# Kernel optimization log

Hardware: AMD Instinct MI355X
Metric: run time of the kernel (lower is better)

## Reference

```python
import jax, jax.numpy as jnp
import numpy as np

N_LAYERS = 12
N_CH = 256
N_IN = 4
KS = 3
SPECT_CH = 640


def conv1d(x, w, b, dilation):
    # x: [B, T, Cin], w: [K, Cin, Cout] (WIO), SAME padding, given dilation
    y = jax.lax.conv_general_dilated(
        x, w, window_strides=(1,), padding='SAME',
        rhs_dilation=(dilation,), dimension_numbers=('NWC', 'WIO', 'NWC'))
    return y + b


def setup_inputs() -> dict:
    key = jax.random.key(0)
    ks = jax.random.split(key, 16)
    s = 0.02
    inp = {}
    inp['audio'] = jax.random.normal(ks[0], (8, 4096, N_IN), dtype=jnp.float32)
    inp['spect'] = jax.random.normal(ks[1], (8, 4096, SPECT_CH), dtype=jnp.float32)
    # start 1x1 conv: [Cin, Cout]
    inp['w_start'] = jax.random.normal(ks[2], (N_IN, N_CH), dtype=jnp.float32) * s
    inp['b_start'] = jnp.zeros((N_CH,), dtype=jnp.float32)
    # dilated in_layers: stacked [L, K, Cin, 2*Cout]
    inp['w_in'] = jax.random.normal(ks[3], (N_LAYERS, KS, N_CH, 2 * N_CH), dtype=jnp.float32) * s
    inp['b_in'] = jnp.zeros((N_LAYERS, 2 * N_CH), dtype=jnp.float32)
    # cond 1x1 convs: stacked [L, SPECT_CH, 2*Cout]
    inp['w_cond'] = jax.random.normal(ks[4], (N_LAYERS, SPECT_CH, 2 * N_CH), dtype=jnp.float32) * s
    inp['b_cond'] = jnp.zeros((N_LAYERS, 2 * N_CH), dtype=jnp.float32)
    # res_skip 1x1 convs: first L-1 have 2*Cout, last has Cout
    inp['w_res'] = jax.random.normal(ks[5], (N_LAYERS - 1, N_CH, 2 * N_CH), dtype=jnp.float32) * s
    inp['b_res'] = jnp.zeros((N_LAYERS - 1, 2 * N_CH), dtype=jnp.float32)
    inp['w_res_last'] = jax.random.normal(ks[6], (N_CH, N_CH), dtype=jnp.float32) * s
    inp['b_res_last'] = jnp.zeros((N_CH,), dtype=jnp.float32)
    # end 1x1 conv (zero-initialized in the original; use small random for a
    # non-degenerate numerical baseline)
    inp['w_end'] = jax.random.normal(ks[7], (N_CH, 2 * N_IN), dtype=jnp.float32) * s
    inp['b_end'] = jnp.zeros((2 * N_IN,), dtype=jnp.float32)
    return inp


def reference(audio, spect, w_start, b_start, w_in, b_in, w_cond, b_cond,
              w_res, b_res, w_res_last, b_res_last, w_end, b_end):
    # start: 1x1 conv == matmul over channels
    started = jnp.einsum('btc,cd->btd', audio, w_start) + b_start  # [B,T,256]
    # precompute all conditioning projections: [L,B,T,512]
    cond_all = jnp.einsum('btc,lcd->lbtd', spect, w_cond) + b_cond[:, None, None, :]
    output = None
    for i in range(N_LAYERS):
        in_l = conv1d(started, w_in[i], b_in[i], 2 ** i)  # [B,T,512]
        acts = in_l + cond_all[i]
        half_tanh = jnp.tanh(acts[..., :N_CH])
        half_sig = jax.nn.sigmoid(acts[..., N_CH:])
        activated = half_tanh * half_sig  # [B,T,256]
        if i < N_LAYERS - 1:
            rs = jnp.einsum('btc,cd->btd', activated, w_res[i]) + b_res[i]
            started = started + rs[..., :N_CH]
            skip = rs[..., N_CH:]
        else:
            skip = jnp.einsum('btc,cd->btd', activated, w_res_last) + b_res_last
        output = skip if output is None else output + skip
    out = jnp.einsum('btc,cd->btd', output, w_end) + b_end  # [B,T,2*N_IN]
    return out
```

## Files before the change

### kernel.cpp

```cpp
#include <hip/hip_runtime.h>
#include <cstdint>

#define PAD 2048
#define KG 1408

typedef float f32x4 __attribute__((ext_vector_type(4)));
typedef __bf16 bf16x8 __attribute__((ext_vector_type(8)));
typedef __bf16 bf16x4 __attribute__((ext_vector_type(4)));

__device__ __forceinline__ void g2l16(const void* g, void* l) {
    __builtin_amdgcn_global_load_lds(
        (__attribute__((address_space(1))) void*)(uintptr_t)g,
        (__attribute__((address_space(3))) void*)(uint32_t)(uintptr_t)l,
        16, 0, 0);
}


__global__ void cvt_bf16_kernel(const float4* __restrict__ src, bf16x4* __restrict__ dst, int n4) {
    int idx = blockIdx.x * 256 + threadIdx.x;
    if (idx < n4) {
        float4 v = src[idx];
        bf16x4 o = {(__bf16)v.x, (__bf16)v.y, (__bf16)v.z, (__bf16)v.w};
        dst[idx] = o;
    }
}

__global__ void init_started_kernel(const float* __restrict__ audio, const float* __restrict__ w_start,
                                    const float* __restrict__ b_start, __bf16* __restrict__ started_pad) {
    int pr = blockIdx.x * 4 + (threadIdx.x >> 6);
    int c0 = (threadIdx.x & 63) * 4;
    int off = pr & 8191;
    bf16x4 o = {(__bf16)0.f, (__bf16)0.f, (__bf16)0.f, (__bf16)0.f};
    if (off >= PAD && off < PAD + 4096) {
        int r = ((pr >> 13) << 12) + (off - PAD);
        float a0 = audio[r * 4 + 0], a1 = audio[r * 4 + 1], a2 = audio[r * 4 + 2], a3 = audio[r * 4 + 3];
        for (int j = 0; j < 4; ++j) {
            int c = c0 + j;
            o[j] = (__bf16)(b_start[c] + a0 * w_start[c] + a1 * w_start[256 + c]
                            + a2 * w_start[512 + c] + a3 * w_start[768 + c]);
        }
    }
    *(bf16x4*)&started_pad[(size_t)pr * 256 + c0] = o;
}

__global__ void transpose_gate(const float* __restrict__ w_in, const float* __restrict__ w_cond,
                               __bf16* __restrict__ Wg) {
    __shared__ float tile[64][65];
    int i = blockIdx.z;
    int k0 = blockIdx.y * 64, n0 = blockIdx.x * 64;
    int tid = threadIdx.x, c = tid & 63, rr = tid >> 6;
    for (int it = 0; it < 16; ++it) {
        int kl = it * 4 + rr;
        int k = k0 + kl;
        int np = n0 + c;
        int phys = ((np >> 4) & 1) * 256 + (np >> 5) * 16 + (np & 15);
        float v;
        if (k < 768) v = w_in[((i * 3 + (k >> 8)) * 256 + (k & 255)) * 512 + phys];
        else         v = w_cond[(i * 640 + (k - 768)) * 512 + phys];
        tile[kl][c] = v;
    }
    __syncthreads();
    for (int it = 0; it < 16; ++it) {
        int nl = it * 4 + rr;
        Wg[(size_t)(i * 512 + n0 + nl) * KG + k0 + c] = (__bf16)tile[c][nl];
    }
}

__global__ void transpose_kn(const float* __restrict__ src, __bf16* __restrict__ dst,
                             int K, int N, int srcLS, int dstLS) {
    __shared__ float tile[64][65];
    int i = blockIdx.z;
    int k0 = blockIdx.y * 64, n0 = blockIdx.x * 64;
    int tid = threadIdx.x, c = tid & 63, rr = tid >> 6;
    const float* s = src + (size_t)i * srcLS;
    __bf16* dp = dst + (size_t)i * dstLS;
    for (int it = 0; it < 16; ++it) {
        int kl = it * 4 + rr;
        tile[kl][c] = s[(k0 + kl) * N + n0 + c];
    }
    __syncthreads();
    for (int it = 0; it < 16; ++it) {
        int nl = it * 4 + rr;
        dp[(size_t)(n0 + nl) * K + k0 + c] = (__bf16)tile[c][nl];
    }
}

__global__ void bias_gate_kernel(const float* __restrict__ b_in, const float* __restrict__ b_cond,
                                 float* __restrict__ bias) {
    int idx = blockIdx.x * 256 + threadIdx.x;
    int i = idx >> 9, np = idx & 511;
    int phys = ((np >> 4) & 1) * 256 + (np >> 5) * 16 + (np & 15);
    bias[idx] = b_in[i * 512 + phys] + b_cond[i * 512 + phys];
}

__global__ void wfold_kernel(const float* __restrict__ w_res, const float* __restrict__ w_res_last,
                             const float* __restrict__ w_end, const float* __restrict__ b_res,
                             const float* __restrict__ b_res_last, const float* __restrict__ b_end,
                             float* __restrict__ wfold, float* __restrict__ outconst) {
    if (blockIdx.x == 96) {
        __shared__ float red[256][8];
        int j = threadIdx.x;
        float bsum = b_res_last[j];
        for (int i = 0; i < 11; ++i) bsum += b_res[i * 512 + 256 + j];
        for (int c = 0; c < 8; ++c) red[j][c] = bsum * w_end[j * 8 + c];
        __syncthreads();
        if (j < 8) {
            float s = b_end[j];
            for (int t = 0; t < 256; ++t) s += red[t][j];
            outconst[j] = s;
        }
        return;
    }
    int idx = blockIdx.x * 256 + threadIdx.x;
    int i = idx >> 11, rem = idx & 2047, k = rem >> 3, c = rem & 7;
    float s = 0.f;
    if (i < 11) {
        const float* wr = w_res + (size_t)(i * 256 + k) * 512 + 256;
        for (int j = 0; j < 256; ++j) s += wr[j] * w_end[j * 8 + c];
    } else {
        const float* wr = w_res_last + k * 256;
        for (int j = 0; j < 256; ++j) s += wr[j] * w_end[j * 8 + c];
    }
    wfold[idx] = s;
}


__global__ __launch_bounds__(256) void gate_kernel(
    const __bf16* __restrict__ started_pad, const __bf16* __restrict__ spect,
    const __bf16* __restrict__ Wg,
    const float* __restrict__ bias,
    __bf16* __restrict__ activated, int d) {
    __shared__ __align__(16) __bf16 S[4][128 * 32];
    const int tid = threadIdx.x;
    const int m0 = blockIdx.x * 128;
    const int n0 = blockIdx.y * 128;
    const int padbase = ((m0 >> 12) << 13) + PAD + (m0 & 4095);
    const int srow = tid >> 2;
    const int skq = (tid & 3) * 8;
    const int wave = tid >> 6, lane = tid & 63;
    const int wm = (wave >> 1) * 64, wn = (wave & 1) * 64;
    const int quad = lane >> 4, l15 = lane & 15;

    f32x4 acc[4][4];
    for (int i = 0; i < 4; i++)
        for (int j = 0; j < 4; j++) acc[i][j] = f32x4{0.f, 0.f, 0.f, 0.f};

    const __bf16* Bbase = Wg + (n0 + srow) * KG + skq;

    bf16x8 rA0, rA1, rB0, rB1;
    auto loadTile = [&](int kk) {
        const __bf16* gA0;
        int rstride;
        if (kk < 768) {
            int tap = kk >> 8;
            int koff = kk & 255;
            gA0 = started_pad + (padbase + srow + (tap - 1) * d) * 256 + koff + skq;
            rstride = 256;
        } else {
            gA0 = spect + (m0 + srow) * 640 + (kk - 768) + skq;
            rstride = 640;
        }
        rA0 = *(const bf16x8*)gA0;
        rA1 = *(const bf16x8*)(gA0 + 64 * rstride);
        const __bf16* gB0 = Bbase + kk;
        rB0 = *(const bf16x8*)gB0;
        rB1 = *(const bf16x8*)(gB0 + 64 * KG);
    };

    loadTile(0);
    *(bf16x8*)&S[0][srow * 32 + skq] = rA0;
    *(bf16x8*)&S[0][(64 + srow) * 32 + skq] = rA1;
    *(bf16x8*)&S[2][srow * 32 + skq] = rB0;
    *(bf16x8*)&S[2][(64 + srow) * 32 + skq] = rB1;
    loadTile(32);
    __syncthreads();

    for (int ks = 0; ks < 44; ++ks) {
        const int cur = ks & 1, nxt = cur ^ 1;
        bf16x8 a[4], b[4];
        for (int mi = 0; mi < 4; mi++) a[mi] = *(const bf16x8*)&S[cur][(wm + mi * 16 + l15) * 32 + quad * 8];
        for (int ni = 0; ni < 4; ni++) b[ni] = *(const bf16x8*)&S[2 + cur][(wn + ni * 16 + l15) * 32 + quad * 8];
        if (ks + 1 < 44) {
            *(bf16x8*)&S[nxt][srow * 32 + skq] = rA0;
            *(bf16x8*)&S[nxt][(64 + srow) * 32 + skq] = rA1;
            *(bf16x8*)&S[2 + nxt][srow * 32 + skq] = rB0;
            *(bf16x8*)&S[2 + nxt][(64 + srow) * 32 + skq] = rB1;
        }
        if (ks + 2 < 44) loadTile((ks + 2) * 32);
        for (int mi = 0; mi < 4; mi++)
            for (int ni = 0; ni < 4; ni++)
                acc[mi][ni] = __builtin_amdgcn_mfma_f32_16x16x32_bf16(a[mi], b[ni], acc[mi][ni], 0, 0, 0);
        __syncthreads();
    }

    __bf16* tile = &S[0][0];
    int chloc0 = (wn >> 1) + l15;
    for (int nj = 0; nj < 2; ++nj) {
        int colT = wn + nj * 32 + l15;
        float bt = bias[n0 + colT];
        float bs = bias[n0 + colT + 16];
        int chl = chloc0 + nj * 16;
        for (int mi = 0; mi < 4; ++mi) {
            for (int reg = 0; reg < 4; ++reg) {
                int row = wm + mi * 16 + quad * 4 + reg;
                float xt = acc[mi][2 * nj][reg] + bt;
                float xs = acc[mi][2 * nj + 1][reg] + bs;
                float th = 2.f / (1.f + __expf(-2.f * xt)) - 1.f;
                float sg = 1.f / (1.f + __expf(-xs));
                tile[row * 68 + chl] = (__bf16)(th * sg);
            }
        }
    }
    __syncthreads();
    int rowb = tid >> 3, seg = tid & 7;
    int chb = n0 >> 1;
    for (int j = 0; j < 4; ++j) {
        int row = rowb + 32 * j;
        bf16x8 v = *(const bf16x8*)&tile[row * 68 + seg * 8];
        *(bf16x8*)&activated[(m0 + row) * 256 + chb + seg * 8] = v;
    }
}

__global__ __launch_bounds__(256) void res_kernel(
    const __bf16* __restrict__ activated, const __bf16* __restrict__ Wr,
    const float* __restrict__ b_res,
    const float* __restrict__ wfold,
    const float* __restrict__ outconst,
    __bf16* __restrict__ started_pad, float* __restrict__ out, int initOut) {
    __shared__ __align__(16) __bf16 As[128 * 32];
    __shared__ __align__(16) __bf16 Bs[128 * 32];
    __shared__ __align__(16) float Wf[2048];
    const int tid = threadIdx.x;
    const int m0 = blockIdx.x * 128;
    const int n0 = blockIdx.y * 128;
    const int srow = tid >> 2;
    const int skq = (tid & 3) * 8;
    const int wave = tid >> 6, lane = tid & 63;
    const int wm = (wave >> 1) * 64, wn = (wave & 1) * 64;
    const int quad = lane >> 4, l15 = lane & 15;
    const bool doOut = (blockIdx.y == 0);
    const int row2 = tid >> 1, half = tid & 1;

    if (doOut) {
        float4* wf4 = (float4*)Wf;
        const float4* src4 = (const float4*)wfold;
        wf4[tid] = src4[tid];
        wf4[256 + tid] = src4[256 + tid];
    }

    f32x4 acc[4][4];
    for (int i = 0; i < 4; i++)
        for (int j = 0; j < 4; j++) acc[i][j] = f32x4{0.f, 0.f, 0.f, 0.f};
    float ox = 0.f, oy = 0.f, oz = 0.f, ow = 0.f;

    const __bf16* Abase = activated + (m0 + srow) * 256 + skq;
    const __bf16* Bbase = Wr + (n0 + srow) * 256 + skq;

    for (int ks = 0; ks < 8; ++ks) {
        int kk = ks * 32;
        g2l16(Abase + kk, &As[srow * 32 + skq]);
        g2l16(Abase + kk + 64 * 256, &As[(64 + srow) * 32 + skq]);
        g2l16(Bbase + kk, &Bs[srow * 32 + skq]);
        g2l16(Bbase + kk + 64 * 256, &Bs[(64 + srow) * 32 + skq]);
        __syncthreads();
        bf16x8 a[4], b[4];
        for (int mi = 0; mi < 4; mi++) a[mi] = *(const bf16x8*)&As[(wm + mi * 16 + l15) * 32 + quad * 8];
        for (int ni = 0; ni < 4; ni++) b[ni] = *(const bf16x8*)&Bs[(wn + ni * 16 + l15) * 32 + quad * 8];
        for (int mi = 0; mi < 4; mi++)
            for (int ni = 0; ni < 4; ni++)
                acc[mi][ni] = __builtin_amdgcn_mfma_f32_16x16x32_bf16(a[mi], b[ni], acc[mi][ni], 0, 0, 0);
        if (doOut) {
            const bf16x8* ap = (const bf16x8*)&As[row2 * 32];
            const float4* wf = (const float4*)Wf;
            for (int c8 = 0; c8 < 4; ++c8) {
                bf16x8 av = ap[c8];
                int kb = (kk + c8 * 8) * 2 + half;
                for (int e = 0; e < 8; ++e) {
                    float a = (float)av[e];
                    float4 w = wf[kb + e * 2];
                    ox += a * w.x; oy += a * w.y; oz += a * w.z; ow += a * w.w;
                }
            }
        }
        __syncthreads();
    }

    for (int ni = 0; ni < 4; ++ni) {
        int col = n0 + wn + ni * 16 + l15;
        float bcol = b_res[col];
        for (int mi = 0; mi < 4; ++mi) {
            for (int reg = 0; reg < 4; ++reg) {
                int r = m0 + wm + mi * 16 + quad * 4 + reg;
                int pr = ((r >> 12) << 13) + PAD + (r & 4095);
                int idx = pr * 256 + col;
                float f = (float)started_pad[idx] + acc[mi][ni][reg] + bcol;
                started_pad[idx] = (__bf16)f;
            }
        }
    }
    if (doOut) {
        int r = m0 + row2;
        float4* op = (float4*)&out[r * 8 + half * 4];
        float4 o;
        if (initOut) {
            float4 oc = ((const float4*)outconst)[half];
            o.x = oc.x + ox; o.y = oc.y + oy; o.z = oc.z + oz; o.w = oc.w + ow;
        } else {
            o = *op;
            o.x += ox; o.y += oy; o.z += oz; o.w += ow;
        }
        *op = o;
    }
}

__global__ __launch_bounds__(256) void outacc_kernel(
    const __bf16* __restrict__ activated, const float* __restrict__ wfold,
    float* __restrict__ out) {
    __shared__ __align__(16) float Wf[2048];
    int tid = threadIdx.x;
    ((float4*)Wf)[tid] = ((const float4*)wfold)[tid];
    ((float4*)Wf)[256 + tid] = ((const float4*)wfold)[256 + tid];
    __syncthreads();
    int row2 = tid >> 1, half = tid & 1;
    int r = blockIdx.x * 128 + row2;
    const bf16x8* ap = (const bf16x8*)(activated + r * 256);
    const float4* wf = (const float4*)Wf;
    float ox = 0.f, oy = 0.f, oz = 0.f, ow = 0.f;
    for (int c8 = 0; c8 < 32; ++c8) {
        bf16x8 av = ap[c8];
        for (int e = 0; e < 8; ++e) {
            float a = (float)av[e];
            float4 w = wf[(c8 * 8 + e) * 2 + half];
            ox += a * w.x; oy += a * w.y; oz += a * w.z; ow += a * w.w;
        }
    }
    float4* op = (float4*)&out[r * 8 + half * 4];
    float4 o = *op;
    o.x += ox; o.y += oy; o.z += oz; o.w += ow;
    *op = o;
}


extern "C" void kernel_launch(void* const* d_in, const int* in_sizes, int n_in,
                              void* d_out, int out_size, void* d_ws, size_t ws_size,
                              hipStream_t stream) {
    const float* audio      = (const float*)d_in[0];
    const float* spect      = (const float*)d_in[1];
    const float* w_start    = (const float*)d_in[2];
    const float* b_start    = (const float*)d_in[3];
    const float* w_in       = (const float*)d_in[4];
    const float* b_in       = (const float*)d_in[5];
    const float* w_cond     = (const float*)d_in[6];
    const float* b_cond     = (const float*)d_in[7];
    const float* w_res      = (const float*)d_in[8];
    const float* b_res      = (const float*)d_in[9];
    const float* w_res_last = (const float*)d_in[10];
    const float* b_res_last = (const float*)d_in[11];
    const float* w_end      = (const float*)d_in[12];
    const float* b_end      = (const float*)d_in[13];
    float* out = (float*)d_out;

    char* ws = (char*)d_ws;
    __bf16* started_pad = (__bf16*)ws; ws += 33554432;
    __bf16* activated   = (__bf16*)ws; ws += 16777216;
    __bf16* spect_bf    = (__bf16*)ws; ws += 41943040;
    __bf16* Wg          = (__bf16*)ws; ws += 17301504;
    __bf16* Wr          = (__bf16*)ws; ws += 1441792;
    float*  wfold       = (float*)ws;  ws += 98304;
    float*  biasg       = (float*)ws;  ws += 24576;
    float*  outconst    = (float*)ws;  ws += 256;

    init_started_kernel<<<dim3(16384), 256, 0, stream>>>(audio, w_start, b_start, started_pad);
    cvt_bf16_kernel<<<dim3(20480), 256, 0, stream>>>((const float4*)spect, (bf16x4*)spect_bf, 5242880);
    transpose_gate<<<dim3(8, 22, 12), 256, 0, stream>>>(w_in, w_cond, Wg);
    transpose_kn<<<dim3(4, 4, 11), 256, 0, stream>>>(w_res, Wr, 256, 512, 256 * 512, 256 * 256);
    bias_gate_kernel<<<dim3(24), 256, 0, stream>>>(b_in, b_cond, biasg);
    wfold_kernel<<<dim3(97), 256, 0, stream>>>(w_res, w_res_last, w_end, b_res, b_res_last, b_end,
                                               wfold, outconst);

    for (int i = 0; i < 12; ++i) {
        gate_kernel<<<dim3(256, 4), 256, 0, stream>>>(
            started_pad, spect_bf, Wg + (size_t)i * 512 * KG, biasg + i * 512, activated, 1 << i);
        if (i < 11) {
            res_kernel<<<dim3(256, 2), 256, 0, stream>>>(
                activated, Wr + (size_t)i * 256 * 256, b_res + i * 512,
                wfold + i * 2048, outconst, started_pad, out, i == 0 ? 1 : 0);
        } else {
            outacc_kernel<<<dim3(256), 256, 0, stream>>>(activated, wfold + 11 * 2048, out);
        }
    }
}
```

Measured before the change: 1.268 ms.

## Widen gate GEMM tile to 128x256 and move output projection onto MFMA

The gate kernel now computes a 128x256 output tile per block, with 8 N-fragments per wave. This halves the number of blocks and reuses each A tile (started/spect) across twice as many columns, cutting redundant A loads. The cost is more accumulator registers and more shared memory, and launch_bounds now asks for 2 blocks per CU. Separately, the folded output projection in res_kernel is done with bf16 MFMA on the two waves with wn==0, replacing the scalar fp32 FMA loop, which trades fp32 weights for bf16 ones.

Measured after the change: 1.098 ms. 13.5% less time.

```diff
diff --git a/kernel.cpp b/kernel.cpp
--- a/kernel.cpp
+++ b/kernel.cpp
@@ -125,29 +125,29 @@
 }
 
 
-__global__ __launch_bounds__(256) void gate_kernel(
+__global__ __launch_bounds__(256, 2) void gate_kernel(
     const __bf16* __restrict__ started_pad, const __bf16* __restrict__ spect,
     const __bf16* __restrict__ Wg,
     const float* __restrict__ bias,
     __bf16* __restrict__ activated, int d) {
-    __shared__ __align__(16) __bf16 S[4][128 * 32];
+    __shared__ __align__(16) __bf16 SMEM[24576];
     const int tid = threadIdx.x;
     const int m0 = blockIdx.x * 128;
-    const int n0 = blockIdx.y * 128;
+    const int n0 = blockIdx.y * 256;
     const int padbase = ((m0 >> 12) << 13) + PAD + (m0 & 4095);
     const int srow = tid >> 2;
     const int skq = (tid & 3) * 8;
     const int wave = tid >> 6, lane = tid & 63;
-    const int wm = (wave >> 1) * 64, wn = (wave & 1) * 64;
+    const int wm = (wave >> 1) * 64, wn = (wave & 1) * 128;
     const int quad = lane >> 4, l15 = lane & 15;
 
-    f32x4 acc[4][4];
+    f32x4 acc[4][8];
     for (int i = 0; i < 4; i++)
-        for (int j = 0; j < 4; j++) acc[i][j] = f32x4{0.f, 0.f, 0.f, 0.f};
+        for (int j = 0; j < 8; j++) acc[i][j] = f32x4{0.f, 0.f, 0.f, 0.f};
 
     const __bf16* Bbase = Wg + (n0 + srow) * KG + skq;
 
-    bf16x8 rA0, rA1, rB0, rB1;
+    bf16x8 rA[2], rB[4];
     auto loadTile = [&](int kk) {
         const __bf16* gA0;
         int rstride;
@@ -160,46 +160,51 @@
             gA0 = spect + (m0 + srow) * 640 + (kk - 768) + skq;
             rstride = 640;
         }
-        rA0 = *(const bf16x8*)gA0;
-        rA1 = *(const bf16x8*)(gA0 + 64 * rstride);
+        rA[0] = *(const bf16x8*)gA0;
+        rA[1] = *(const bf16x8*)(gA0 + 64 * rstride);
         const __bf16* gB0 = Bbase + kk;
-        rB0 = *(const bf16x8*)gB0;
-        rB1 = *(const bf16x8*)(gB0 + 64 * KG);
+        rB[0] = *(const bf16x8*)gB0;
+        rB[1] = *(const bf16x8*)(gB0 + 64 * KG);
+        rB[2] = *(const bf16x8*)(gB0 + 128 * KG);
+        rB[3] = *(const bf16x8*)(gB0 + 192 * KG);
     };
+    auto stash = [&](int buf) {
+        __bf16* Ab = SMEM + buf * 4096;
+        __bf16* Bb = SMEM + 8192 + buf * 8192;
+        *(bf16x8*)&Ab[srow * 32 + skq] = rA[0];
+        *(bf16x8*)&Ab[(64 + srow) * 32 + skq] = rA[1];
+        *(bf16x8*)&Bb[srow * 32 + skq] = rB[0];
+        *(bf16x8*)&Bb[(64 + srow) * 32 + skq] = rB[1];
+        *(bf16x8*)&Bb[(128 + srow) * 32 + skq] = rB[2];
+        *(bf16x8*)&Bb[(192 + srow) * 32 + skq] = rB[3];
+    };
 
     loadTile(0);
-    *(bf16x8*)&S[0][srow * 32 + skq] = rA0;
-    *(bf16x8*)&S[0][(64 + srow) * 32 + skq] = rA1;
-    *(bf16x8*)&S[2][srow * 32 + skq] = rB0;
-    *(bf16x8*)&S[2][(64 + srow) * 32 + skq] = rB1;
+    stash(0);
     loadTile(32);
     __syncthreads();
 
     for (int ks = 0; ks < 44; ++ks) {
         const int cur = ks & 1, nxt = cur ^ 1;
-        bf16x8 a[4], b[4];
-        for (int mi = 0; mi < 4; mi++) a[mi] = *(const bf16x8*)&S[cur][(wm + mi * 16 + l15) * 32 + quad * 8];
-        for (int ni = 0; ni < 4; ni++) b[ni] = *(const bf16x8*)&S[2 + cur][(wn + ni * 16 + l15) * 32 + quad * 8];
-        if (ks + 1 < 44) {
-            *(bf16x8*)&S[nxt][srow * 32 + skq] = rA0;
-            *(bf16x8*)&S[nxt][(64 + srow) * 32 + skq] = rA1;
-            *(bf16x8*)&S[2 + nxt][srow * 32 + skq] = rB0;
-            *(bf16x8*)&S[2 + nxt][(64 + srow) * 32 + skq] = rB1;
-        }
+        const __bf16* Ab = SMEM + cur * 4096;
+        const __bf16* Bb = SMEM + 8192 + cur * 8192;
+        bf16x8 a[4], b[8];
+        for (int mi = 0; mi < 4; mi++) a[mi] = *(const bf16x8*)&Ab[(wm + mi * 16 + l15) * 32 + quad * 8];
+        for (int ni = 0; ni < 8; ni++) b[ni] = *(const bf16x8*)&Bb[(wn + ni * 16 + l15) * 32 + quad * 8];
+        if (ks + 1 < 44) stash(nxt);
         if (ks + 2 < 44) loadTile((ks + 2) * 32);
         for (int mi = 0; mi < 4; mi++)
-            for (int ni = 0; ni < 4; ni++)
+            for (int ni = 0; ni < 8; ni++)
                 acc[mi][ni] = __builtin_amdgcn_mfma_f32_16x16x32_bf16(a[mi], b[ni], acc[mi][ni], 0, 0, 0);
         __syncthreads();
     }
 
-    __bf16* tile = &S[0][0];
-    int chloc0 = (wn >> 1) + l15;
-    for (int nj = 0; nj < 2; ++nj) {
+    __bf16* tile = SMEM;
+    for (int nj = 0; nj < 4; ++nj) {
         int colT = wn + nj * 32 + l15;
         float bt = bias[n0 + colT];
         float bs = bias[n0 + colT + 16];
-        int chl = chloc0 + nj * 16;
+        int chl = (wn >> 1) + nj * 16 + l15;
         for (int mi = 0; mi < 4; ++mi) {
             for (int reg = 0; reg < 4; ++reg) {
                 int row = wm + mi * 16 + quad * 4 + reg;
@@ -207,16 +212,16 @@
                 float xs = acc[mi][2 * nj + 1][reg] + bs;
                 float th = 2.f / (1.f + __expf(-2.f * xt)) - 1.f;
                 float sg = 1.f / (1.f + __expf(-xs));
-                tile[row * 68 + chl] = (__bf16)(th * sg);
+                tile[row * 132 + chl] = (__bf16)(th * sg);
             }
         }
     }
     __syncthreads();
-    int rowb = tid >> 3, seg = tid & 7;
     int chb = n0 >> 1;
-    for (int j = 0; j < 4; ++j) {
-        int row = rowb + 32 * j;
-        bf16x8 v = *(const bf16x8*)&tile[row * 68 + seg * 8];
+    for (int pass = 0; pass < 8; ++pass) {
+        int row = (tid >> 4) + 16 * pass;
+        int seg = tid & 15;
+        bf16x8 v = *(const bf16x8*)&tile[row * 132 + seg * 8];
         *(bf16x8*)&activated[(m0 + row) * 256 + chb + seg * 8] = v;
     }
 }
@@ -229,7 +234,7 @@
     __bf16* __restrict__ started_pad, float* __restrict__ out, int initOut) {
     __shared__ __align__(16) __bf16 As[128 * 32];
     __shared__ __align__(16) __bf16 Bs[128 * 32];
-    __shared__ __align__(16) float Wf[2048];
+    __shared__ __align__(16) __bf16 WfB[16 * 264];
     const int tid = threadIdx.x;
     const int m0 = blockIdx.x * 128;
     const int n0 = blockIdx.y * 128;
@@ -239,22 +244,24 @@
     const int wm = (wave >> 1) * 64, wn = (wave & 1) * 64;
     const int quad = lane >> 4, l15 = lane & 15;
     const bool doOut = (blockIdx.y == 0);
-    const int row2 = tid >> 1, half = tid & 1;
-
-    if (doOut) {
-        float4* wf4 = (float4*)Wf;
-        const float4* src4 = (const float4*)wfold;
-        wf4[tid] = src4[tid];
-        wf4[256 + tid] = src4[256 + tid];
-    }
+    const bool outWave = doOut && (wn == 0);
 
     f32x4 acc[4][4];
     for (int i = 0; i < 4; i++)
         for (int j = 0; j < 4; j++) acc[i][j] = f32x4{0.f, 0.f, 0.f, 0.f};
-    float ox = 0.f, oy = 0.f, oz = 0.f, ow = 0.f;
+    f32x4 acc_o[4];
+    for (int i = 0; i < 4; i++) acc_o[i] = f32x4{0.f, 0.f, 0.f, 0.f};
 
     const __bf16* Abase = activated + (m0 + srow) * 256 + skq;
     const __bf16* Bbase = Wr + (n0 + srow) * 256 + skq;
+
+    if (doOut) {
+        for (int t = 0; t < 16; ++t) {
+            int e = t * 256 + tid;
+            int col = e >> 8, k = e & 255;
+            WfB[col * 264 + k] = (col < 8) ? (__bf16)wfold[k * 8 + col] : (__bf16)0.f;
+        }
+    }
 
     for (int ks = 0; ks < 8; ++ks) {
         int kk = ks * 32;
@@ -269,18 +276,10 @@
         for (int mi = 0; mi < 4; mi++)
             for (int ni = 0; ni < 4; ni++)
                 acc[mi][ni] = __builtin_amdgcn_mfma_f32_16x16x32_bf16(a[mi], b[ni], acc[mi][ni], 0, 0, 0);
-        if (doOut) {
-            const bf16x8* ap = (const bf16x8*)&As[row2 * 32];
-            const float4* wf = (const float4*)Wf;
-            for (int c8 = 0; c8 < 4; ++c8) {
-                bf16x8 av = ap[c8];
-                int kb = (kk + c8 * 8) * 2 + half;
-                for (int e = 0; e < 8; ++e) {
-                    float a = (float)av[e];
-                    float4 w = wf[kb + e * 2];
-                    ox += a * w.x; oy += a * w.y; oz += a * w.z; ow += a * w.w;
-                }
-            }
+        if (outWave) {
+            bf16x8 bx = *(const bf16x8*)&WfB[l15 * 264 + kk + quad * 8];
+            for (int mi = 0; mi < 4; mi++)
+                acc_o[mi] = __builtin_amdgcn_mfma_f32_16x16x32_bf16(a[mi], bx, acc_o[mi], 0, 0, 0);
         }
         __syncthreads();
     }
@@ -298,18 +297,14 @@
             }
         }
     }
-    if (doOut) {
-        int r = m0 + row2;
-        float4* op = (float4*)&out[r * 8 + half * 4];
-        float4 o;
-        if (initOut) {
-            float4 oc = ((const float4*)outconst)[half];
-            o.x = oc.x + ox; o.y = oc.y + oy; o.z = oc.z + oz; o.w = oc.w + ow;
-        } else {
-            o = *op;
-            o.x += ox; o.y += oy; o.z += oz; o.w += ow;
-        }
-        *op = o;
+    if (outWave && l15 < 8) {
+        for (int mi = 0; mi < 4; ++mi) {
+            for (int reg = 0; reg < 4; ++reg) {
+                int r = m0 + wm + mi * 16 + quad * 4 + reg;
+                float base = initOut ? outconst[l15] : out[r * 8 + l15];
+                out[r * 8 + l15] = base + acc_o[mi][reg];
+            }
+        }
     }
 }
 
@@ -379,7 +374,7 @@
                                                wfold, outconst);
 
     for (int i = 0; i < 12; ++i) {
-        gate_kernel<<<dim3(256, 4), 256, 0, stream>>>(
+        gate_kernel<<<dim3(256, 2), 256, 0, stream>>>(
             started_pad, spect_bf, Wg + (size_t)i * 512 * KG, biasg + i * 512, activated, 1 << i);
         if (i < 11) {
             res_kernel<<<dim3(256, 2), 256, 0, stream>>>(
```
